# Optimization experiments

Hardware: AMD Instinct MI355X
Metric: run time of the kernel (lower is better)

The kernel has to match this reference:

```python
import jax, jax.numpy as jnp
import numpy as np


def _conv(x, k, b):
    # x: [B,C,H,W], k: [O,I,kh,kw] torch-style, padding='same'
    y = jax.lax.conv_general_dilated(x, k, window_strides=(1, 1), padding='SAME',
                                     dimension_numbers=('NCHW', 'OIHW', 'NCHW'))
    return y + b[None, :, None, None]


def _chan_linear(x, W, b):
    # torch: transpose(1,3) -> Linear -> transpose(1,3) == linear over channel dim
    # x: [B,C,H,W], W: [C,D] -> [B,D,H,W]
    return jnp.einsum('bchw,cd->bdhw', x, W) + b[None, :, None, None]


def _forward(enc_in, dec_in, eWf, ebf, eWi, ebi, eWc, ebc, eWo, ebo,
             dKf, dbf, dKi, dbi, dKc, dbc, dWo, dbo, oK, ob, lW, lb):
    B, Te, Cin, H, W = enc_in.shape
    Hd = eWf.shape[1]
    h0 = jnp.zeros((B, Hd, H, W), enc_in.dtype)
    c0 = jnp.zeros_like(h0)

    def enc_step(carry, xt):
        h, c = carry
        xc = jnp.concatenate([xt, h], axis=1)  # [B, Cin+Hd, H, W]
        f = jax.nn.sigmoid(_chan_linear(xc, eWf, ebf))
        i = jax.nn.sigmoid(_chan_linear(xc, eWi, ebi))
        g = jnp.tanh(_chan_linear(xc, eWc, ebc))
        o = jax.nn.sigmoid(_chan_linear(xc, eWo, ebo))
        c = c * f + i * g
        h = jnp.tanh(c) * o
        return (h, c), None

    (h, c), _ = jax.lax.scan(enc_step, (h0, c0), jnp.moveaxis(enc_in, 1, 0))

    def dec_step(carry, xt):
        h, c = carry
        xc = jnp.concatenate([xt, h], axis=1)  # [B, Cout+Hd, H, W]
        f = jax.nn.sigmoid(_conv(xc, dKf, dbf))
        i = jax.nn.sigmoid(_conv(xc, dKi, dbi))
        g = jnp.tanh(_conv(xc, dKc, dbc))
        o = jax.nn.sigmoid(_chan_linear(xc, dWo, dbo))
        c = c * f + i * g
        h = jnp.tanh(c) * o
        rho = _conv(h, oK, ob)            # [B, Cout+Hd, H, W]
        rho = _chan_linear(rho, lW, lb)   # [B, Cout, H, W]
        return (h, c), rho

    (_, _), outs = jax.lax.scan(dec_step, (h, c), jnp.moveaxis(dec_in, 1, 0))
    return jnp.moveaxis(outs, 0, 1)  # [B, Td, Cout, H, W]


def setup_inputs() -> dict:
    key = jax.random.key(0)
    ks = jax.random.split(key, 24)
    Cin, Hd, Cout, K = 16, 96, 8, 3
    Ce = Cin + Hd   # 112, encoder concat channels
    Cd = Cout + Hd  # 104, decoder concat channels

    def rn(k, shape, fan_in):
        return jax.random.normal(k, shape, dtype=jnp.float32) * (1.0 / np.sqrt(fan_in))

    z = lambda n: jnp.zeros((n,), jnp.float32)
    return {
        'enc_in': jax.random.normal(ks[0], (8, 12, Cin, 64, 64), jnp.float32),
        'dec_in': jax.random.normal(ks[1], (8, 12, Cout, 64, 64), jnp.float32),
        'eWf': rn(ks[2], (Ce, Hd), Ce), 'ebf': z(Hd),
        'eWi': rn(ks[3], (Ce, Hd), Ce), 'ebi': z(Hd),
        'eWc': rn(ks[4], (Ce, Hd), Ce), 'ebc': z(Hd),
        'eWo': rn(ks[5], (Ce, Hd), Ce), 'ebo': z(Hd),
        'dKf': rn(ks[6], (Hd, Cd, K, K), Cd * K * K), 'dbf': z(Hd),
        'dKi': rn(ks[7], (Hd, Cd, K, K), Cd * K * K), 'dbi': z(Hd),
        'dKc': rn(ks[8], (Hd, Cd, K, K), Cd * K * K), 'dbc': z(Hd),
        'dWo': rn(ks[9], (Cd, Hd), Cd), 'dbo': z(Hd),
        'oK': rn(ks[10], (Cd, Hd, K, K), Hd * K * K), 'ob': z(Cd),
        'lW': rn(ks[11], (Cd, Cout), Cd), 'lb': z(Cout),
    }


def reference(enc_in, dec_in, eWf, ebf, eWi, ebi, eWc, ebc, eWo, ebo,
              dKf, dbf, dKi, dbi, dKc, dbc, dWo, dbo, oK, ob, lW, lb):
    return _forward(enc_in, dec_in, eWf, ebf, eWi, ebi, eWc, ebc, eWo, ebo,
                    dKf, dbf, dKi, dbi, dKc, dbc, dWo, dbo, oK, ob, lW, lb)
```

## Files before the change

kernel.cpp:

```cpp
#include <hip/hip_runtime.h>
#include <hip/hip_bf16.h>

#define B_   8
#define T_   12
#define CIN  16
#define HD   96
#define COUT 8
#define CE   112
#define CD   104
#define HW   4096
#define WIMG 64

typedef __hip_bfloat16 bf16;
typedef __attribute__((ext_vector_type(8))) short bf16x8;
typedef __attribute__((ext_vector_type(16))) float f32x16;
typedef __attribute__((ext_vector_type(4))) int i32x4;

__device__ __forceinline__ float b2f(bf16 v) { return __bfloat162float(v); }
__device__ __forceinline__ float sigmf_(float x) { return 1.0f / (1.0f + __expf(-x)); }
__device__ __forceinline__ float tanhf_(float x) { return 2.0f / (1.0f + __expf(-2.0f * x)) - 1.0f; }

__device__ __forceinline__ float ldin(const void* p, long i, int f32) {
    return f32 ? ((const float*)p)[i] : b2f(((const bf16*)p)[i]);
}
__device__ __forceinline__ short f2bs(float v) {
    __hip_bfloat16 hv = __float2bfloat16(v);
    return *reinterpret_cast<short*>(&hv);
}

__device__ __forceinline__ void mfma_a(f32x16& acc, bf16x8 a, bf16x8 b) {
    asm("v_mfma_f32_32x32x16_bf16 %0, %1, %2, %0"
        : "+a"(acc) : "v"(a), "v"(b));
}

__device__ __forceinline__ i32x4 ldB16(const short* p) {
    i32x4 r;
    asm volatile("global_load_dwordx4 %0, %1, off sc0 sc1"
                 : "=v"(r) : "v"(p) : "memory");
    return r;
}
__device__ __forceinline__ void stB16(short* p, i32x4 v) {
    asm volatile("global_store_dwordx4 %0, %1, off sc0 sc1"
                 :: "v"(p), "v"(v) : "memory");
}
__device__ __forceinline__ void vm0() {
    asm volatile("s_waitcnt vmcnt(0)" ::: "memory");
}

__device__ __forceinline__ void wait_prog(const int* p, int need) {
    while (__hip_atomic_load(p, __ATOMIC_RELAXED, __HIP_MEMORY_SCOPE_AGENT) < need)
        __builtin_amdgcn_s_sleep(1);
}

__device__ __forceinline__ int detect_flag(const void* w) {
    const unsigned short* u = (const unsigned short*)w;
    int bad = 0;
    for (int i = 0; i < 64; i++) {
        unsigned short v = u[i];
        unsigned e = (v >> 7) & 0xFF;
        if (!(v == 0 || (e >= 90 && e <= 128))) bad++;
    }
    return (bad > 8) ? 1 : 0;
}

__global__ void setup_k(
    const void* eWf, const void* ebf_, const void* eWi, const void* ebi_,
    const void* eWc, const void* ebc_, const void* eWo, const void* ebo_,
    const void* dKf, const void* dbf_, const void* dKi, const void* dbi_,
    const void* dKc, const void* dbc_, const void* dWo, const void* dbo_,
    const void* oK,  const void* obv,  const void* lW,  const void* lb,
    float* __restrict__ biases, float* __restrict__ b2,
    short* __restrict__ EW, short* __restrict__ WtA, short* __restrict__ K2A,
    int* __restrict__ flag, int* __restrict__ prog)
{
    const int f = detect_flag(eWf);
    const int bid = blockIdx.x, tid = threadIdx.x;

    if (bid < 3) {
        int idx = bid * 256 + tid;
        if (idx < 768) {
            const void* srcs[8] = {ebf_, ebi_, ebc_, ebo_, dbf_, dbi_, dbc_, dbo_};
            biases[idx] = ldin(srcs[idx / 96], idx % 96, f);
        }
        return;
    }
    if (bid == 3) {
        if (tid < COUT) {
            float a = ldin(lb, tid, f);
            for (int cd = 0; cd < CD; cd++)
                a = fmaf(ldin(obv, cd, f), ldin(lW, cd * COUT + tid, f), a);
            b2[tid] = a;
        }
        if (tid == 32) *flag = f;
        return;
    }
    if (bid == 4) {
        __hip_atomic_store(&prog[tid * 16], 0, __ATOMIC_RELAXED, __HIP_MEMORY_SCOPE_AGENT);
        return;
    }
    if (bid < 26) {
        int lin = (bid - 5) * 256 + tid;
        if (lin >= 7 * 12 * 64) return;
        int lane = lin & 63;
        int rest = lin >> 6;
        int mt = rest % 12;
        int k0 = rest / 12;
        int m = mt * 32 + (lane & 31);
        int gate = m / 96, d = m % 96;
        int chb = k0 * 16 + (lane >> 5) * 8;
        const void* W = (gate == 0) ? eWf : (gate == 1) ? eWi : (gate == 2) ? eWc : eWo;
        #pragma unroll
        for (int j = 0; j < 8; j++)
            EW[(size_t)lin * 8 + j] = f2bs(ldin(W, (size_t)(chb + j) * HD + d, f));
        return;
    }
    if (bid < 215) {
        int lin = (bid - 26) * 256 + tid;
        if (lin >= 9 * 7 * 12 * 64) return;
        int lane = lin & 63;
        int rest = lin >> 6;
        int mt  = rest % 12;
        int k07 = rest / 12;
        int k0  = k07 % 7;
        int tap = k07 / 7;
        int m = mt * 32 + (lane & 31);
        int gate = m / 96, d = m % 96;
        int chb = k0 * 16 + (lane >> 5) * 8;
        #pragma unroll
        for (int j = 0; j < 8; j++) {
            int ch = chb + j;
            float v = 0.f;
            if (ch < 104) {
                long ki = ((long)d * CD + ch) * 9 + tap;
                if (gate == 0)      v = ldin(dKf, ki, f);
                else if (gate == 1) v = ldin(dKi, ki, f);
                else if (gate == 2) v = ldin(dKc, ki, f);
                else                v = (tap == 4) ? ldin(dWo, (long)ch * HD + d, f) : 0.f;
            }
            WtA[(size_t)lin * 8 + j] = f2bs(v);
        }
        return;
    }
    {
        int lin = (bid - 215) * 256 + tid;
        if (lin >= 9 * 7 * 64) return;
        int lane = lin & 63;
        int rest = lin >> 6;
        int k0 = rest % 7;
        int tap = rest / 7;
        int m = lane & 31;
        int kb = k0 * 16 + (lane >> 5) * 8;
        #pragma unroll 1
        for (int j = 0; j < 8; j++) {
            int c = kb + j - 8;
            float v = 0.f;
            if (m < 8 && c >= 0 && c < 96) {
                long i = (long)c * 9 + tap;
                for (int cd = 0; cd < CD; cd++)
                    v = fmaf(ldin(oK, (long)cd * (HD * 9) + i, f),
                             ldin(lW, (long)cd * COUT + m, f), v);
            }
            K2A[(size_t)lin * 8 + j] = f2bs(v);
        }
    }
}

__device__ __forceinline__ void ldfragsD(bf16x8* A, bf16x8& K, bf16x8& B,
                                         const short* ab, const short* kb,
                                         const short* rec, int k0, int kj, int ldA)
{
    const short* a0 = ab + (size_t)k0 * 12 * 64 * 8;
    if (ldA) {
        #pragma unroll
        for (int mt = 0; mt < 9; mt++)
            A[mt] = *(const bf16x8*)(a0 + (size_t)mt * 512);
    }
    K = *(const bf16x8*)(kb + (size_t)k0 * 512);
    B = *(const bf16x8*)(rec + k0 * 16 + kj * 8);
}

__global__ void __launch_bounds__(256, 1) net_k(
    const void* __restrict__ xe, const void* __restrict__ xd,
    short* __restrict__ hPA, short* __restrict__ hPB,
    void* __restrict__ out,
    const short* __restrict__ EW, const short* __restrict__ WtA,
    const short* __restrict__ K2A,
    const float* __restrict__ ebf, const float* __restrict__ ebi,
    const float* __restrict__ ebc, const float* __restrict__ ebo,
    const float* __restrict__ dbf, const float* __restrict__ dbi,
    const float* __restrict__ dbc, const float* __restrict__ dbo,
    const float* __restrict__ b2, const int* __restrict__ flag,
    int* __restrict__ prog)
{
    __shared__ short lds[4 * 66 * 120];
    const int f32 = *flag;
    const int tid  = threadIdx.x;
    const int b    = blockIdx.x & 7;
    const int band = blockIdx.x >> 3;
    const int y0   = band * 2;
    const int pix0 = y0 * 64;
    const int wave = tid >> 6, lane = tid & 63;
    const int n = lane & 31, kj = lane >> 5;
    const int px = wave * 32 + n;
    const int pg = pix0 + px;
    const i32x4 z4 = {0, 0, 0, 0};

    float cre[48];
    #pragma unroll
    for (int i = 0; i < 48; i++) cre[i] = 0.f;

    #pragma unroll 1
    for (int t = 0; t < T_; t++) {
        #pragma unroll
        for (int it = 0; it < 2; it++) {
            int i = tid + it * 256;
            int ch = i & 15, q = i >> 4;
            size_t base = ((size_t)(b * T_ + t) * CIN + ch) * HW + pix0 + q * 4;
            short v0, v1, v2, v3;
            if (f32) {
                float4 f = *(const float4*)((const float*)xe + base);
                v0 = f2bs(f.x); v1 = f2bs(f.y); v2 = f2bs(f.z); v3 = f2bs(f.w);
            } else {
                short4 sv = *(const short4*)((const short*)xe + base);
                v0 = sv.x; v1 = sv.y; v2 = sv.z; v3 = sv.w;
            }
            int sb = q * 4;
            lds[(sb + 0) * 120 + ch] = v0;
            lds[(sb + 1) * 120 + ch] = v1;
            lds[(sb + 2) * 120 + ch] = v2;
            lds[(sb + 3) * 120 + ch] = v3;
        }
        __syncthreads();

        f32x16 acc[12];
        #pragma unroll
        for (int m = 0; m < 12; m++)
            #pragma unroll
            for (int r = 0; r < 16; r++) acc[m][r] = 0.f;

        const short* rec = &lds[px * 120];
        if (t == 0) {
            bf16x8 cB = *(const bf16x8*)(rec + kj * 8);
            #pragma unroll
            for (int mt = 0; mt < 12; mt++) {
                bf16x8 a = *(const bf16x8*)(EW + ((size_t)mt * 64 + lane) * 8);
                mfma_a(acc[mt], a, cB);
            }
        } else {
            bf16x8 cA[12], cB;
            cB = *(const bf16x8*)(rec + kj * 8);
            #pragma unroll
            for (int mt = 0; mt < 12; mt++)
                cA[mt] = *(const bf16x8*)(EW + ((size_t)mt * 64 + lane) * 8);
            #pragma unroll
            for (int k0 = 0; k0 < 7; k0++) {
                bf16x8 nA[12], nB;
                if (k0 < 6) {
                    nB = *(const bf16x8*)(rec + (k0 + 1) * 16 + kj * 8);
                    #pragma unroll
                    for (int mt = 0; mt < 12; mt++)
                        nA[mt] = *(const bf16x8*)(EW + ((size_t)((k0 + 1) * 12 + mt) * 64 + lane) * 8);
                }
                #pragma unroll
                for (int mt = 0; mt < 12; mt++) mfma_a(acc[mt], cA[mt], cB);
                if (k0 < 6) {
                    #pragma unroll
                    for (int mt = 0; mt < 12; mt++) cA[mt] = nA[mt];
                    cB = nB;
                }
            }
        }
        __syncthreads();

        #pragma unroll
        for (int dt = 0; dt < 3; dt++) {
            #pragma unroll
            for (int r = 0; r < 16; r++) {
                int row = (r & 3) + 8 * (r >> 2) + 4 * kj;
                int d = dt * 32 + row;
                float fg = sigmf_(acc[dt][r]     + ebf[d]);
                float ig = sigmf_(acc[3 + dt][r] + ebi[d]);
                float gg = tanhf_(acc[6 + dt][r] + ebc[d]);
                float og = sigmf_(acc[9 + dt][r] + ebo[d]);
                int ci = dt * 16 + r;
                float cn = fmaf(cre[ci], fg, ig * gg);
                cre[ci] = cn;
                lds[px * 120 + 16 + d] = f2bs(tanhf_(cn) * og);
            }
        }
        __syncthreads();
        if (t == T_ - 1) {
            int px2 = tid >> 1, half = tid & 1;
            short* gdst = hPA + ((size_t)b * HW + pix0 + px2) * 96 + half * 48;
            const short* lsrc = &lds[px2 * 120 + 16 + half * 48];
            #pragma unroll
            for (int s2 = 0; s2 < 6; s2++)
                stB16(gdst + s2 * 8, *(const i32x4*)(lsrc + s2 * 8));
        }
    }
    vm0();
    __syncthreads();
    if (tid == 0)
        __hip_atomic_store(&prog[blockIdx.x * 16], 1, __ATOMIC_RELAXED, __HIP_MEMORY_SCOPE_AGENT);

    #pragma unroll 1
    for (int tt = 0; tt <= T_; tt++) {
        short* hR  = (tt & 1) ? hPB : hPA;
        short* hWr = (tt & 1) ? hPA : hPB;

        if (tt == 0) {
            #pragma unroll 1
            for (int i = tid; i < 648; i += 256) {
                int addr_sh;
                if (i < 120) {
                    int r = i / 30, rem = i % 30;
                    int s = (rem / 15) * 65;
                    addr_sh = (r * 66 + s) * 120 + (rem % 15) * 8;
                } else {
                    int z = i - 120;
                    addr_sh = (z >> 1) * 120 + 104 + (z & 1) * 8;
                }
                *(i32x4*)(&lds[addr_sh]) = z4;
            }
        }
        if (tt < T_) {
            #pragma unroll
            for (int it = 0; it < 2; it++) {
                int i = tid + it * 256;
                int ch = i & 7, q = (i >> 3) & 15, r = i >> 7;
                int y = y0 - 1 + r;
                short v0 = 0, v1 = 0, v2 = 0, v3 = 0;
                if ((unsigned)y < 64u) {
                    size_t base = ((size_t)(b * T_ + tt) * COUT + ch) * HW + y * 64 + q * 4;
                    if (f32) {
                        float4 f = *(const float4*)((const float*)xd + base);
                        v0 = f2bs(f.x); v1 = f2bs(f.y); v2 = f2bs(f.z); v3 = f2bs(f.w);
                    } else {
                        short4 sv = *(const short4*)((const short*)xd + base);
                        v0 = sv.x; v1 = sv.y; v2 = sv.z; v3 = sv.w;
                    }
                }
                int sb = r * 66 + 1 + q * 4;
                lds[(sb + 0) * 120 + ch] = v0;
                lds[(sb + 1) * 120 + ch] = v1;
                lds[(sb + 2) * 120 + ch] = v2;
                lds[(sb + 3) * 120 + ch] = v3;
            }
        }

        if (tid < 2) {
            int nb = band + (tid ? 1 : -1);
            if ((unsigned)nb < 32u)
                wait_prog(prog + (((nb << 3) | b) << 4), tt + 1);
        }
        __syncthreads();

        if (tt == 0) {
            i32x4 tmp[12]; int ss2[12], jj2[12];
            #pragma unroll
            for (int i = 0; i < 12; i++) {
                int c2 = tid + i * 256;
                int s = c2 / 12, j = c2 - s * 12;
                ss2[i] = s; jj2[i] = j;
                int y = y0 - 1 + (s >> 6);
                if ((unsigned)y < 64u)
                    tmp[i] = ldB16(hR + ((size_t)b * HW + (size_t)y * 64 + (s & 63)) * 96 + j * 8);
                else tmp[i] = z4;
            }
            vm0();
            #pragma unroll
            for (int i = 0; i < 12; i++) {
                int s = ss2[i];
                *(i32x4*)(&lds[((s >> 6) * 66 + 1 + (s & 63)) * 120 + 8 + jj2[i] * 8]) = tmp[i];
            }
        } else {
            i32x4 tmp[6]; int ss2[6], jj2[6];
            #pragma unroll
            for (int i = 0; i < 6; i++) {
                int c2 = tid + i * 256;
                int s = c2 / 12, j = c2 - s * 12;
                int hi = s >> 6;
                int y = hi ? (y0 + 2) : (y0 - 1);
                ss2[i] = hi * 3 * 66 + 1 + (s & 63);
                jj2[i] = j;
                if ((unsigned)y < 64u)
                    tmp[i] = ldB16(hR + ((size_t)b * HW + (size_t)y * 64 + (s & 63)) * 96 + j * 8);
                else tmp[i] = z4;
            }
            vm0();
            #pragma unroll
            for (int i = 0; i < 6; i++)
                *(i32x4*)(&lds[ss2[i] * 120 + 8 + jj2[i] * 8]) = tmp[i];
        }
        __syncthreads();

        const int rw = 1 + (wave >> 1);
        const int x0 = (wave & 1) * 32;
        const int ldA = (tt < T_) ? 1 : 0;

        f32x16 aF[9], aO[3], aOut;
        #pragma unroll
        for (int m = 0; m < 9; m++)
            #pragma unroll
            for (int r = 0; r < 16; r++) aF[m][r] = 0.f;
        #pragma unroll
        for (int m = 0; m < 3; m++)
            #pragma unroll
            for (int r = 0; r < 16; r++) aO[m][r] = 0.f;
        #pragma unroll
        for (int r = 0; r < 16; r++) aOut[r] = 0.f;

        {
            bf16x8 cA[9], cK, cB;
            {
                const short* rec0 = &lds[((rw - 1) * 66 + x0 + n) * 120];
                ldfragsD(cA, cK, cB, WtA + (size_t)lane * 8, K2A + (size_t)lane * 8,
                         rec0, 0, kj, ldA);
            }
            #pragma unroll 1
            for (int tap = 0; tap < 9; tap++) {
                int dy = tap / 3 - 1, dx = tap - (tap / 3) * 3 - 1;
                int tapN = (tap < 8) ? tap + 1 : 8;
                int dyN = tapN / 3 - 1, dxN = tapN - (tapN / 3) * 3 - 1;
                const short* rec  = &lds[((rw + dy)  * 66 + 1 + x0 + n + dx)  * 120];
                const short* recN = &lds[((rw + dyN) * 66 + 1 + x0 + n + dxN) * 120];
                const short* ab  = WtA + ((size_t)(tap  * 7) * 12 * 64 + lane) * 8;
                const short* abN = WtA + ((size_t)(tapN * 7) * 12 * 64 + lane) * 8;
                const short* kb  = K2A + ((size_t)(tap  * 7) * 64 + lane) * 8;
                const short* kbN = K2A + ((size_t)(tapN * 7) * 64 + lane) * 8;
                #pragma unroll
                for (int k0 = 0; k0 < 7; k0++) {
                    bf16x8 nA[9], nK, nB;
                    if (k0 < 6) ldfragsD(nA, nK, nB, ab, kb, rec, k0 + 1, kj, ldA);
                    else        ldfragsD(nA, nK, nB, abN, kbN, recN, 0, kj, ldA);
                    if (tt < T_) {
                        #pragma unroll
                        for (int mt = 0; mt < 9; mt++) mfma_a(aF[mt], cA[mt], cB);
                    }
                    if (tt > 0) mfma_a(aOut, cK, cB);
                    #pragma unroll
                    for (int q = 0; q < 9; q++) cA[q] = nA[q];
                    cK = nK; cB = nB;
                }
            }
        }
        if (tt < T_) {
            const short* rec = &lds[(rw * 66 + 1 + x0 + n) * 120];
            const short* ab = WtA + ((size_t)(4 * 7) * 12 * 64 + lane) * 8 + 9 * 512;
            bf16x8 cA[3], cB;
            cB = *(const bf16x8*)(rec + kj * 8);
            #pragma unroll
            for (int mt = 0; mt < 3; mt++)
                cA[mt] = *(const bf16x8*)(ab + (size_t)mt * 512);
            #pragma unroll
            for (int k0 = 0; k0 < 7; k0++) {
                bf16x8 nA[3], nB;
                if (k0 < 6) {
                    const short* a0 = ab + (size_t)(k0 + 1) * 12 * 64 * 8;
                    nB = *(const bf16x8*)(rec + (k0 + 1) * 16 + kj * 8);
                    #pragma unroll
                    for (int mt = 0; mt < 3; mt++)
                        nA[mt] = *(const bf16x8*)(a0 + (size_t)mt * 512);
                }
                #pragma unroll
                for (int mt = 0; mt < 3; mt++) mfma_a(aO[mt], cA[mt], cB);
                if (k0 < 6) {
                    #pragma unroll
                    for (int mt = 0; mt < 3; mt++) cA[mt] = nA[mt];
                    cB = nB;
                }
            }
        }
        __syncthreads();

        if (tt > 0) {
            #pragma unroll
            for (int r = 0; r < 4; r++) {
                int o = r + 4 * kj;
                float v = aOut[r] + b2[o];
                size_t oadr = ((size_t)(b * T_ + (tt - 1)) * COUT + o) * HW + pg;
                if (f32) ((float*)out)[oadr] = v;
                else     ((bf16*)out)[oadr] = __float2bfloat16(v);
            }
        }

        if (tt < T_) {
            #pragma unroll
            for (int dt = 0; dt < 3; dt++) {
                #pragma unroll
                for (int r = 0; r < 16; r++) {
                    int row = (r & 3) + 8 * (r >> 2) + 4 * kj;
                    int d = dt * 32 + row;
                    float fg = sigmf_(aF[dt][r]     + dbf[d]);
                    float ig = sigmf_(aF[3 + dt][r] + dbi[d]);
                    float gg = tanhf_(aF[6 + dt][r] + dbc[d]);
                    float og = sigmf_(aO[dt][r]     + dbo[d]);
                    int ci = dt * 16 + r;
                    float cn = fmaf(cre[ci], fg, ig * gg);
                    cre[ci] = cn;
                    float hv = tanhf_(cn) * og;
                    lds[((1 + (px >> 6)) * 66 + 1 + (px & 63)) * 120 + 8 + d] = f2bs(hv);
                }
            }
            __syncthreads();
            int px2 = tid >> 1, half = tid & 1;
            short* gdst = hWr + ((size_t)b * HW + pix0 + px2) * 96 + half * 48;
            const short* lsrc = &lds[((1 + (px2 >> 6)) * 66 + 1 + (px2 & 63)) * 120 + 8 + half * 48];
            #pragma unroll
            for (int s2 = 0; s2 < 6; s2++)
                stB16(gdst + s2 * 8, *(const i32x4*)(lsrc + s2 * 8));
            vm0();
            __syncthreads();
            if (tid == 0)
                __hip_atomic_store(&prog[blockIdx.x * 16], tt + 2,
                                   __ATOMIC_RELAXED, __HIP_MEMORY_SCOPE_AGENT);
        }
    }
}

extern "C" void kernel_launch(void* const* d_in, const int* in_sizes, int n_in,
                              void* d_out, int out_size, void* d_ws, size_t ws_size,
                              hipStream_t stream)
{
    const void* enc_in = d_in[0];
    const void* dec_in = d_in[1];
    const void* eWf = d_in[2];  const void* ebf_ = d_in[3];
    const void* eWi = d_in[4];  const void* ebi_ = d_in[5];
    const void* eWc = d_in[6];  const void* ebc_ = d_in[7];
    const void* eWo = d_in[8];  const void* ebo_ = d_in[9];
    const void* dKf = d_in[10]; const void* dbf_ = d_in[11];
    const void* dKi = d_in[12]; const void* dbi_ = d_in[13];
    const void* dKc = d_in[14]; const void* dbc_ = d_in[15];
    const void* dWo = d_in[16]; const void* dbo_ = d_in[17];
    const void* oK  = d_in[18]; const void* obv = d_in[19];
    const void* lW  = d_in[20]; const void* lb  = d_in[21];

    int* flag = (int*)d_ws;
    int* prog = (int*)d_ws + 16;
    float* ws = (float*)d_ws + 16 + 4096;

    const int S = B_ * HD * HW;
    short* hPA = (short*)ws;
    short* hPB = (short*)(ws + S / 2);
    float* biases = ws + S;
    float* b2   = biases + 768;
    short* WtA  = (short*)(b2 + 16);
    short* EW   = (short*)(b2 + 16 + 193536);
    short* K2A  = (short*)(b2 + 16 + 193536 + 21504);

    setup_k<<<dim3(231), dim3(256), 0, stream>>>(
        eWf, ebf_, eWi, ebi_, eWc, ebc_, eWo, ebo_,
        dKf, dbf_, dKi, dbi_, dKc, dbc_, dWo, dbo_,
        oK, obv, lW, lb,
        biases, b2, EW, WtA, K2A, flag, prog);

    net_k<<<dim3(256), dim3(256), 0, stream>>>(
        enc_in, dec_in, hPA, hPB, d_out,
        EW, WtA, K2A,
        biases + 0, biases + 96, biases + 192, biases + 288,
        biases + 384, biases + 480, biases + 576, biases + 672,
        b2, flag, prog);
}
```

Before: 1.047 ms.

## Split gate MFMA work across two wave groups with 512-thread blocks

```diff
diff --git a/kernel.cpp b/kernel.cpp
--- a/kernel.cpp
+++ b/kernel.cpp
@@ -10,6 +10,10 @@
 #define CD   104
 #define HW   4096
 #define WIMG 64
+
+#define TILE_SH 31680
+#define XG_F    12416
+#define LDS_BYTES (63360 + 2 * XG_F * 4)
 
 typedef __hip_bfloat16 bf16;
 typedef __attribute__((ext_vector_type(8))) short bf16x8;
@@ -165,21 +169,7 @@
     }
 }
 
-__device__ __forceinline__ void ldfragsD(bf16x8* A, bf16x8& K, bf16x8& B,
-                                         const short* ab, const short* kb,
-                                         const short* rec, int k0, int kj, int ldA)
-{
-    const short* a0 = ab + (size_t)k0 * 12 * 64 * 8;
-    if (ldA) {
-        #pragma unroll
-        for (int mt = 0; mt < 9; mt++)
-            A[mt] = *(const bf16x8*)(a0 + (size_t)mt * 512);
-    }
-    K = *(const bf16x8*)(kb + (size_t)k0 * 512);
-    B = *(const bf16x8*)(rec + k0 * 16 + kj * 8);
-}
-
-__global__ void __launch_bounds__(256, 1) net_k(
+__global__ void __launch_bounds__(512, 2) net_k(
     const void* __restrict__ xe, const void* __restrict__ xd,
     short* __restrict__ hPA, short* __restrict__ hPB,
     void* __restrict__ out,
@@ -192,7 +182,9 @@
     const float* __restrict__ b2, const int* __restrict__ flag,
     int* __restrict__ prog)
 {
-    __shared__ short lds[4 * 66 * 120];
+    extern __shared__ short lds[];
+    float* xg = (float*)(lds + TILE_SH);
+    float* xo = xg + XG_F;
     const int f32 = *flag;
     const int tid  = threadIdx.x;
     const int b    = blockIdx.x & 7;
@@ -200,8 +192,10 @@
     const int y0   = band * 2;
     const int pix0 = y0 * 64;
     const int wave = tid >> 6, lane = tid & 63;
+    const int grp  = wave >> 2;
+    const int wv   = wave & 3;
     const int n = lane & 31, kj = lane >> 5;
-    const int px = wave * 32 + n;
+    const int px = wv * 32 + n;
     const int pg = pix0 + px;
     const i32x4 z4 = {0, 0, 0, 0};
 
@@ -211,10 +205,8 @@
 
     #pragma unroll 1
     for (int t = 0; t < T_; t++) {
-        #pragma unroll
-        for (int it = 0; it < 2; it++) {
-            int i = tid + it * 256;
-            int ch = i & 15, q = i >> 4;
+        {
+            int ch = tid & 15, q = tid >> 4;
             size_t base = ((size_t)(b * T_ + t) * CIN + ch) * HW + pix0 + q * 4;
             short v0, v1, v2, v3;
             if (f32) {
@@ -232,70 +224,80 @@
         }
         __syncthreads();
 
-        f32x16 acc[12];
+        f32x16 acc[6];
         #pragma unroll
-        for (int m = 0; m < 12; m++)
+        for (int m = 0; m < 6; m++)
             #pragma unroll
             for (int r = 0; r < 16; r++) acc[m][r] = 0.f;
 
         const short* rec = &lds[px * 120];
+        const int mt0 = grp * 6;
         if (t == 0) {
             bf16x8 cB = *(const bf16x8*)(rec + kj * 8);
             #pragma unroll
-            for (int mt = 0; mt < 12; mt++) {
-                bf16x8 a = *(const bf16x8*)(EW + ((size_t)mt * 64 + lane) * 8);
-                mfma_a(acc[mt], a, cB);
-            }
+            for (int m = 0; m < 6; m++)
+                mfma_a(acc[m], *(const bf16x8*)(EW + (size_t)(mt0 + m) * 512 + lane * 8), cB);
         } else {
-            bf16x8 cA[12], cB;
+            bf16x8 cA[6], cB;
             cB = *(const bf16x8*)(rec + kj * 8);
             #pragma unroll
-            for (int mt = 0; mt < 12; mt++)
-                cA[mt] = *(const bf16x8*)(EW + ((size_t)mt * 64 + lane) * 8);
+            for (int m = 0; m < 6; m++)
+                cA[m] = *(const bf16x8*)(EW + (size_t)(mt0 + m) * 512 + lane * 8);
             #pragma unroll
             for (int k0 = 0; k0 < 7; k0++) {
-                bf16x8 nA[12], nB;
+                bf16x8 nA[6], nB;
                 if (k0 < 6) {
                     nB = *(const bf16x8*)(rec + (k0 + 1) * 16 + kj * 8);
                     #pragma unroll
-                    for (int mt = 0; mt < 12; mt++)
-                        nA[mt] = *(const bf16x8*)(EW + ((size_t)((k0 + 1) * 12 + mt) * 64 + lane) * 8);
-                }
-                #pragma unroll
-                for (int mt = 0; mt < 12; mt++) mfma_a(acc[mt], cA[mt], cB);
+                    for (int m = 0; m < 6; m++)
+                        nA[m] = *(const bf16x8*)(EW + (size_t)((k0 + 1) * 12 + mt0 + m) * 512 + lane * 8);
+                }
+                #pragma unroll
+                for (int m = 0; m < 6; m++) mfma_a(acc[m], cA[m], cB);
                 if (k0 < 6) {
                     #pragma unroll
-                    for (int mt = 0; mt < 12; mt++) cA[mt] = nA[mt];
+                    for (int m = 0; m < 6; m++) cA[m] = nA[m];
                     cB = nB;
                 }
             }
         }
         __syncthreads();
 
-        #pragma unroll
-        for (int dt = 0; dt < 3; dt++) {
-            #pragma unroll
-            for (int r = 0; r < 16; r++) {
-                int row = (r & 3) + 8 * (r >> 2) + 4 * kj;
-                int d = dt * 32 + row;
-                float fg = sigmf_(acc[dt][r]     + ebf[d]);
-                float ig = sigmf_(acc[3 + dt][r] + ebi[d]);
-                float gg = tanhf_(acc[6 + dt][r] + ebc[d]);
-                float og = sigmf_(acc[9 + dt][r] + ebo[d]);
-                int ci = dt * 16 + r;
-                float cn = fmaf(cre[ci], fg, ig * gg);
-                cre[ci] = cn;
-                lds[px * 120 + 16 + d] = f2bs(tanhf_(cn) * og);
-            }
+        if (grp == 1) {
+            #pragma unroll
+            for (int dt = 0; dt < 3; dt++)
+                #pragma unroll
+                for (int r = 0; r < 16; r++) {
+                    int row = (r & 3) + 8 * (r >> 2) + 4 * kj;
+                    int d = dt * 32 + row;
+                    xg[px * 97 + d] = tanhf_(acc[dt][r]     + ebc[d]);
+                    xo[px * 97 + d] = sigmf_(acc[3 + dt][r] + ebo[d]);
+                }
+        }
+        __syncthreads();
+        if (grp == 0) {
+            #pragma unroll
+            for (int dt = 0; dt < 3; dt++)
+                #pragma unroll
+                for (int r = 0; r < 16; r++) {
+                    int row = (r & 3) + 8 * (r >> 2) + 4 * kj;
+                    int d = dt * 32 + row;
+                    float fg = sigmf_(acc[dt][r]     + ebf[d]);
+                    float ig = sigmf_(acc[3 + dt][r] + ebi[d]);
+                    int ci = dt * 16 + r;
+                    float cn = fmaf(cre[ci], fg, ig * xg[px * 97 + d]);
+                    cre[ci] = cn;
+                    lds[px * 120 + 16 + d] = f2bs(tanhf_(cn) * xo[px * 97 + d]);
+                }
         }
         __syncthreads();
         if (t == T_ - 1) {
-            int px2 = tid >> 1, half = tid & 1;
-            short* gdst = hPA + ((size_t)b * HW + pix0 + px2) * 96 + half * 48;
-            const short* lsrc = &lds[px2 * 120 + 16 + half * 48];
-            #pragma unroll
-            for (int s2 = 0; s2 < 6; s2++)
-                stB16(gdst + s2 * 8, *(const i32x4*)(lsrc + s2 * 8));
+            #pragma unroll 1
+            for (int c = tid; c < 1536; c += 512) {
+                int rec2 = c / 12, part = c - (c / 12) * 12;
+                stB16(hPA + ((size_t)b * HW + pix0 + rec2) * 96 + part * 8,
+                      *(const i32x4*)(&lds[rec2 * 120 + 16 + part * 8]));
+            }
         }
     }
     vm0();
@@ -310,7 +312,7 @@
 
         if (tt == 0) {
             #pragma unroll 1
-            for (int i = tid; i < 648; i += 256) {
+            for (int i = tid; i < 648; i += 512) {
                 int addr_sh;
                 if (i < 120) {
                     int r = i / 30, rem = i % 30;
@@ -324,28 +326,24 @@
             }
         }
         if (tt < T_) {
-            #pragma unroll
-            for (int it = 0; it < 2; it++) {
-                int i = tid + it * 256;
-                int ch = i & 7, q = (i >> 3) & 15, r = i >> 7;
-                int y = y0 - 1 + r;
-                short v0 = 0, v1 = 0, v2 = 0, v3 = 0;
-                if ((unsigned)y < 64u) {
-                    size_t base = ((size_t)(b * T_ + tt) * COUT + ch) * HW + y * 64 + q * 4;
-                    if (f32) {
-                        float4 f = *(const float4*)((const float*)xd + base);
-                        v0 = f2bs(f.x); v1 = f2bs(f.y); v2 = f2bs(f.z); v3 = f2bs(f.w);
-                    } else {
-                        short4 sv = *(const short4*)((const short*)xd + base);
-                        v0 = sv.x; v1 = sv.y; v2 = sv.z; v3 = sv.w;
-                    }
-                }
-                int sb = r * 66 + 1 + q * 4;
-                lds[(sb + 0) * 120 + ch] = v0;
-                lds[(sb + 1) * 120 + ch] = v1;
-                lds[(sb + 2) * 120 + ch] = v2;
-                lds[(sb + 3) * 120 + ch] = v3;
-            }
+            int ch = tid & 7, q = (tid >> 3) & 15, r = tid >> 7;
+            int y = y0 - 1 + r;
+            short v0 = 0, v1 = 0, v2 = 0, v3 = 0;
+            if ((unsigned)y < 64u) {
+                size_t base = ((size_t)(b * T_ + tt) * COUT + ch) * HW + y * 64 + q * 4;
+                if (f32) {
+                    float4 f = *(const float4*)((const float*)xd + base);
+                    v0 = f2bs(f.x); v1 = f2bs(f.y); v2 = f2bs(f.z); v3 = f2bs(f.w);
+                } else {
+                    short4 sv = *(const short4*)((const short*)xd + base);
+                    v0 = sv.x; v1 = sv.y; v2 = sv.z; v3 = sv.w;
+                }
+            }
+            int sb = r * 66 + 1 + q * 4;
+            lds[(sb + 0) * 120 + ch] = v0;
+            lds[(sb + 1) * 120 + ch] = v1;
+            lds[(sb + 2) * 120 + ch] = v2;
+            lds[(sb + 3) * 120 + ch] = v3;
         }
 
         if (tid < 2) {
@@ -356,10 +354,10 @@
         __syncthreads();
 
         if (tt == 0) {
-            i32x4 tmp[12]; int ss2[12], jj2[12];
-            #pragma unroll
-            for (int i = 0; i < 12; i++) {
-                int c2 = tid + i * 256;
+            i32x4 tmp[6]; int ss2[6], jj2[6];
+            #pragma unroll
+            for (int i = 0; i < 6; i++) {
+                int c2 = tid + i * 512;
                 int s = c2 / 12, j = c2 - s * 12;
                 ss2[i] = s; jj2[i] = j;
                 int y = y0 - 1 + (s >> 6);
@@ -369,15 +367,15 @@
             }
             vm0();
             #pragma unroll
-            for (int i = 0; i < 12; i++) {
+            for (int i = 0; i < 6; i++) {
                 int s = ss2[i];
                 *(i32x4*)(&lds[((s >> 6) * 66 + 1 + (s & 63)) * 120 + 8 + jj2[i] * 8]) = tmp[i];
             }
         } else {
-            i32x4 tmp[6]; int ss2[6], jj2[6];
-            #pragma unroll
-            for (int i = 0; i < 6; i++) {
-                int c2 = tid + i * 256;
+            i32x4 tmp[3]; int ss2[3], jj2[3];
+            #pragma unroll
+            for (int i = 0; i < 3; i++) {
+                int c2 = tid + i * 512;
                 int s = c2 / 12, j = c2 - s * 12;
                 int hi = s >> 6;
                 int y = hi ? (y0 + 2) : (y0 - 1);
@@ -389,91 +387,122 @@
             }
             vm0();
             #pragma unroll
-            for (int i = 0; i < 6; i++)
+            for (int i = 0; i < 3; i++)
                 *(i32x4*)(&lds[ss2[i] * 120 + 8 + jj2[i] * 8]) = tmp[i];
         }
         __syncthreads();
 
-        const int rw = 1 + (wave >> 1);
-        const int x0 = (wave & 1) * 32;
-        const int ldA = (tt < T_) ? 1 : 0;
-
-        f32x16 aF[9], aO[3], aOut;
-        #pragma unroll
-        for (int m = 0; m < 9; m++)
-            #pragma unroll
-            for (int r = 0; r < 16; r++) aF[m][r] = 0.f;
-        #pragma unroll
-        for (int m = 0; m < 3; m++)
-            #pragma unroll
-            for (int r = 0; r < 16; r++) aO[m][r] = 0.f;
-        #pragma unroll
-        for (int r = 0; r < 16; r++) aOut[r] = 0.f;
-
-        {
-            bf16x8 cA[9], cK, cB;
-            {
-                const short* rec0 = &lds[((rw - 1) * 66 + x0 + n) * 120];
-                ldfragsD(cA, cK, cB, WtA + (size_t)lane * 8, K2A + (size_t)lane * 8,
-                         rec0, 0, kj, ldA);
-            }
+        const int rw = 1 + (wv >> 1);
+        const int x0 = (wv & 1) * 32;
+
+        f32x16 aF[6], aG[3], aOc[3], aOut;
+        if (grp == 0) {
+            #pragma unroll
+            for (int m = 0; m < 6; m++)
+                #pragma unroll
+                for (int r = 0; r < 16; r++) aF[m][r] = 0.f;
+        } else {
+            #pragma unroll
+            for (int m = 0; m < 3; m++)
+                #pragma unroll
+                for (int r = 0; r < 16; r++) { aG[m][r] = 0.f; aOc[m][r] = 0.f; }
+            #pragma unroll
+            for (int r = 0; r < 16; r++) aOut[r] = 0.f;
+        }
+
+        if (grp == 0 && tt < T_) {
+            bf16x8 cA[6], cB;
+            cB = *(const bf16x8*)(&lds[((rw - 1) * 66 + x0 + n) * 120] + kj * 8);
+            #pragma unroll
+            for (int m = 0; m < 6; m++)
+                cA[m] = *(const bf16x8*)(WtA + (size_t)m * 512 + lane * 8);
             #pragma unroll 1
-            for (int tap = 0; tap < 9; tap++) {
-                int dy = tap / 3 - 1, dx = tap - (tap / 3) * 3 - 1;
-                int tapN = (tap < 8) ? tap + 1 : 8;
-                int dyN = tapN / 3 - 1, dxN = tapN - (tapN / 3) * 3 - 1;
-                const short* rec  = &lds[((rw + dy)  * 66 + 1 + x0 + n + dx)  * 120];
-                const short* recN = &lds[((rw + dyN) * 66 + 1 + x0 + n + dxN) * 120];
-                const short* ab  = WtA + ((size_t)(tap  * 7) * 12 * 64 + lane) * 8;
-                const short* abN = WtA + ((size_t)(tapN * 7) * 12 * 64 + lane) * 8;
-                const short* kb  = K2A + ((size_t)(tap  * 7) * 64 + lane) * 8;
-                const short* kbN = K2A + ((size_t)(tapN * 7) * 64 + lane) * 8;
+            for (int u = 0; u < 63; u++) {
+                int un = (u < 62) ? u + 1 : 62;
+                int tapn = un / 7, k0n = un - tapn * 7;
+                int dyn_ = tapn / 3 - 1, dxn = tapn - (tapn / 3) * 3 - 1;
+                bf16x8 nA[6], nB;
+                nB = *(const bf16x8*)(&lds[((rw + dyn_) * 66 + 1 + x0 + n + dxn) * 120]
+                                      + k0n * 16 + kj * 8);
+                #pragma unroll
+                for (int m = 0; m < 6; m++)
+                    nA[m] = *(const bf16x8*)(WtA + ((size_t)un * 12 + m) * 512 + lane * 8);
+                #pragma unroll
+                for (int m = 0; m < 6; m++) mfma_a(aF[m], cA[m], cB);
+                #pragma unroll
+                for (int m = 0; m < 6; m++) cA[m] = nA[m];
+                cB = nB;
+            }
+        }
+        if (grp == 1) {
+            bf16x8 cG[3], cK, cB;
+            cB = *(const bf16x8*)(&lds[((rw - 1) * 66 + x0 + n) * 120] + kj * 8);
+            #pragma unroll
+            for (int m = 0; m < 3; m++)
+                cG[m] = *(const bf16x8*)(WtA + (size_t)(6 + m) * 512 + lane * 8);
+            cK = *(const bf16x8*)(K2A + lane * 8);
+            #pragma unroll 1
+            for (int u = 0; u < 63; u++) {
+                int un = (u < 62) ? u + 1 : 62;
+                int tapn = un / 7, k0n = un - tapn * 7;
+                int dyn_ = tapn / 3 - 1, dxn = tapn - (tapn / 3) * 3 - 1;
+                bf16x8 nG[3], nK, nB;
+                nB = *(const bf16x8*)(&lds[((rw + dyn_) * 66 + 1 + x0 + n + dxn) * 120]
+                                      + k0n * 16 + kj * 8);
+                #pragma unroll
+                for (int m = 0; m < 3; m++)
+                    nG[m] = *(const bf16x8*)(WtA + ((size_t)un * 12 + 6 + m) * 512 + lane * 8);
+                nK = *(const bf16x8*)(K2A + (size_t)un * 512 + lane * 8);
+                if (tt < T_) {
+                    #pragma unroll
+                    for (int m = 0; m < 3; m++) mfma_a(aG[m], cG[m], cB);
+                }
+                if (tt > 0) mfma_a(aOut, cK, cB);
+                #pragma unroll
+                for (int m = 0; m < 3; m++) cG[m] = nG[m];
+                cK = nK; cB = nB;
+            }
+            if (tt < T_) {
+                const short* recc = &lds[(rw * 66 + 1 + x0 + n) * 120];
+                bf16x8 cO[3], cB2 = *(const bf16x8*)(recc + kj * 8);
+                #pragma unroll
+                for (int m = 0; m < 3; m++)
+                    cO[m] = *(const bf16x8*)(WtA + ((size_t)28 * 12 + 9 + m) * 512 + lane * 8);
                 #pragma unroll
                 for (int k0 = 0; k0 < 7; k0++) {
-                    bf16x8 nA[9], nK, nB;
-                    if (k0 < 6) ldfragsD(nA, nK, nB, ab, kb, rec, k0 + 1, kj, ldA);
-                    else        ldfragsD(nA, nK, nB, abN, kbN, recN, 0, kj, ldA);
-                    if (tt < T_) {
+                    bf16x8 nO[3], nB2;
+                    if (k0 < 6) {
+                        nB2 = *(const bf16x8*)(recc + (k0 + 1) * 16 + kj * 8);
                         #pragma unroll
-                        for (int mt = 0; mt < 9; mt++) mfma_a(aF[mt], cA[mt], cB);
+                        for (int m = 0; m < 3; m++)
+                            nO[m] = *(const bf16x8*)(WtA + ((size_t)(29 + k0) * 12 + 9 + m) * 512 + lane * 8);
                     }
-                    if (tt > 0) mfma_a(aOut, cK, cB);
                     #pragma unroll
-                    for (int q = 0; q < 9; q++) cA[q] = nA[q];
-                    cK = nK; cB = nB;
-                }
-            }
-        }
-        if (tt < T_) {
-            const short* rec = &lds[(rw * 66 + 1 + x0 + n) * 120];
-            const short* ab = WtA + ((size_t)(4 * 7) * 12 * 64 + lane) * 8 + 9 * 512;
-            bf16x8 cA[3], cB;
-            cB = *(const bf16x8*)(rec + kj * 8);
-            #pragma unroll
-            for (int mt = 0; mt < 3; mt++)
-                cA[mt] = *(const bf16x8*)(ab + (size_t)mt * 512);
-            #pragma unroll
-            for (int k0 = 0; k0 < 7; k0++) {
-                bf16x8 nA[3], nB;
-                if (k0 < 6) {
-                    const short* a0 = ab + (size_t)(k0 + 1) * 12 * 64 * 8;
-                    nB = *(const bf16x8*)(rec + (k0 + 1) * 16 + kj * 8);
-                    #pragma unroll
-                    for (int mt = 0; mt < 3; mt++)
-                        nA[mt] = *(const bf16x8*)(a0 + (size_t)mt * 512);
-                }
-                #pragma unroll
-                for (int mt = 0; mt < 3; mt++) mfma_a(aO[mt], cA[mt], cB);
-                if (k0 < 6) {
-                    #pragma unroll
-                    for (int mt = 0; mt < 3; mt++) cA[mt] = nA[mt];
-                    cB = nB;
-                }
-            }
-        }
-        __syncthreads();
-
-        if (tt > 0) {
+                    for (int m = 0; m < 3; m++) mfma_a(aOc[m], cO[m], cB2);
+                    if (k0 < 6) {
+                        #pragma unroll
+                        for (int m = 0; m < 3; m++) cO[m] = nO[m];
+                        cB2 = nB2;
+                    }
+                }
+            }
+        }
+        __syncthreads();
+
+        if (grp == 1 && tt < T_) {
+            #pragma unroll
+            for (int dt = 0; dt < 3; dt++)
+                #pragma unroll
+                for (int r = 0; r < 16; r++) {
+                    int row = (r & 3) + 8 * (r >> 2) + 4 * kj;
+                    int d = dt * 32 + row;
+                    xg[px * 97 + d] = tanhf_(aG[dt][r]  + dbc[d]);
+                    xo[px * 97 + d] = sigmf_(aOc[dt][r] + dbo[d]);
+                }
+        }
+        __syncthreads();
+
+        if (grp == 1 && tt > 0) {
             #pragma unroll
             for (int r = 0; r < 4; r++) {
                 int o = r + 4 * kj;
@@ -483,32 +512,32 @@
                 else     ((bf16*)out)[oadr] = __float2bfloat16(v);
             }
         }
-
-        if (tt < T_) {
-            #pragma unroll
-            for (int dt = 0; dt < 3; dt++) {
+        if (grp == 0 && tt < T_) {
+            #pragma unroll
+            for (int dt = 0; dt < 3; dt++)
                 #pragma unroll
                 for (int r = 0; r < 16; r++) {
                     int row = (r & 3) + 8 * (r >> 2) + 4 * kj;
                     int d = dt * 32 + row;
                     float fg = sigmf_(aF[dt][r]     + dbf[d]);
                     float ig = sigmf_(aF[3 + dt][r] + dbi[d]);
-                    float gg = tanhf_(aF[6 + dt][r] + dbc[d]);
-                    float og = sigmf_(aO[dt][r]     + dbo[d]);
                     int ci = dt * 16 + r;
-                    float cn = fmaf(cre[ci], fg, ig * gg);
+                    float cn = fmaf(cre[ci], fg, ig * xg[px * 97 + d]);
                     cre[ci] = cn;
-                    float hv = tanhf_(cn) * og;
-                    lds[((1 + (px >> 6)) * 66 + 1 + (px & 63)) * 120 + 8 + d] = f2bs(hv);
-                }
-            }
-            __syncthreads();
-            int px2 = tid >> 1, half = tid & 1;
-            short* gdst = hWr + ((size_t)b * HW + pix0 + px2) * 96 + half * 48;
-            const short* lsrc = &lds[((1 + (px2 >> 6)) * 66 + 1 + (px2 & 63)) * 120 + 8 + half * 48];
-            #pragma unroll
-            for (int s2 = 0; s2 < 6; s2++)
-                stB16(gdst + s2 * 8, *(const i32x4*)(lsrc + s2 * 8));
+                    lds[((1 + (px >> 6)) * 66 + 1 + (px & 63)) * 120 + 8 + d]
+                        = f2bs(tanhf_(cn) * xo[px * 97 + d]);
+                }
+        }
+        __syncthreads();
+
+        if (tt < T_) {
+            #pragma unroll 1
+            for (int c = tid; c < 1536; c += 512) {
+                int rec2 = c / 12, part = c - (c / 12) * 12;
+                stB16(hWr + ((size_t)b * HW + pix0 + rec2) * 96 + part * 8,
+                      *(const i32x4*)(&lds[((1 + (rec2 >> 6)) * 66 + 1 + (rec2 & 63)) * 120
+                                           + 8 + part * 8]));
+            }
             vm0();
             __syncthreads();
             if (tid == 0)
@@ -548,13 +577,16 @@
     short* EW   = (short*)(b2 + 16 + 193536);
     short* K2A  = (short*)(b2 + 16 + 193536 + 21504);
 
+    hipFuncSetAttribute(reinterpret_cast<const void*>(net_k),
+                        hipFuncAttributeMaxDynamicSharedMemorySize, LDS_BYTES);
+
     setup_k<<<dim3(231), dim3(256), 0, stream>>>(
         eWf, ebf_, eWi, ebi_, eWc, ebc_, eWo, ebo_,
         dKf, dbf_, dKi, dbi_, dKc, dbc_, dWo, dbo_,
         oK, obv, lW, lb,
         biases, b2, EW, WtA, K2A, flag, prog);
 
-    net_k<<<dim3(256), dim3(256), 0, stream>>>(
+    net_k<<<dim3(256), dim3(512), LDS_BYTES, stream>>>(
         enc_in, dec_in, hPA, hPB, d_out,
         EW, WtA, K2A,
         biases + 0, biases + 96, biases + 192, biases + 288,
```

Result: slower. 2.726 ms (+160.4%).
